# Kernel tuning notes

Hardware: AMD Instinct MI355X
Metric: run time of the kernel (lower is better)

## Reference

```python
import jax, jax.numpy as jnp
import numpy as np

D_MODEL = 1024
D_INNER = 2 * D_MODEL
D_STATE = 16
DT_RANK = (D_MODEL + 15) // 16  # math.ceil(d_model/16) = 64
D_CONV = 4
SEQ_L = 2048
BATCH = 2


def setup_inputs() -> dict:
    key = jax.random.key(0)
    ks = jax.random.split(key, 8)
    def w(k, shape, scale=0.02):
        return jax.random.normal(k, shape, dtype=jnp.float32) * scale
    x = jax.random.normal(ks[0], (SEQ_L, BATCH, D_MODEL), dtype=jnp.float32)
    # weights stored as (in, out); torch Linear is x @ W.T with W (out, in)
    W_in = w(ks[1], (D_MODEL, 2 * D_INNER))
    W_conv = w(ks[2], (D_INNER, 1, D_CONV), 0.3)  # depthwise conv kernel (O, I/groups=1, K)
    b_conv = jnp.zeros((D_INNER,), jnp.float32)
    W_x = w(ks[3], (D_INNER, DT_RANK + 2 * D_STATE))
    W_dt = w(ks[4], (DT_RANK, D_INNER))
    b_dt = jnp.zeros((D_INNER,), jnp.float32)
    A_log = jnp.log(jnp.broadcast_to(jnp.arange(1, D_STATE + 1, dtype=jnp.float32),
                                     (D_INNER, D_STATE)))
    D = jnp.ones((D_INNER,), jnp.float32)
    W_out = w(ks[5], (D_INNER, D_MODEL))
    return {"x": x, "W_in": W_in, "W_conv": W_conv, "b_conv": b_conv,
            "W_x": W_x, "W_dt": W_dt, "b_dt": b_dt,
            "A_log": A_log, "D": D, "W_out": W_out}


def _mamba_forward(x, W_in, W_conv, b_conv, W_x, W_dt, b_dt, A_log, D, W_out):
    xb = jnp.transpose(x, (1, 0, 2))                       # (b, l, d_model)
    b, l, _ = xb.shape
    x_and_res = xb @ W_in                                  # (b, l, 2*d_inner)
    xs, res = jnp.split(x_and_res, 2, axis=-1)
    # depthwise causal conv1d: torch pads d_conv-1 both sides then truncates to l
    xc = jnp.transpose(xs, (0, 2, 1))                      # (b, d_inner, l)
    xc = jax.lax.conv_general_dilated(
        xc, W_conv, window_strides=(1,), padding=[(D_CONV - 1, 0)],
        feature_group_count=D_INNER,
        dimension_numbers=("NCH", "OIH", "NCH")) + b_conv[None, :, None]
    u = jax.nn.silu(jnp.transpose(xc, (0, 2, 1)))          # (b, l, d_inner)
    # SSM parameters
    A = -jnp.exp(A_log)                                    # (d_inner, n)
    x_dbl = u @ W_x                                        # (b, l, dt_rank + 2n)
    delta, Bm, Cm = jnp.split(x_dbl, [DT_RANK, DT_RANK + D_STATE], axis=-1)
    delta = jax.nn.softplus(delta @ W_dt + b_dt)           # (b, l, d_inner)
    # selective scan: state (b, d_inner, n)
    def step(state, inp):
        d_t, B_t, C_t, u_t = inp                           # (b,d_in),(b,n),(b,n),(b,d_in)
        dA = jnp.exp(d_t[:, :, None] * A)                  # (b, d_inner, n)
        dBu = d_t[:, :, None] * B_t[:, None, :] * u_t[:, :, None]
        state = dA * state + dBu
        y_t = jnp.einsum("bdn,bn->bd", state, C_t)
        return state, y_t

    init = jnp.zeros((b, D_INNER, D_STATE), jnp.float32)
    seq = (jnp.moveaxis(delta, 1, 0), jnp.moveaxis(Bm, 1, 0),
           jnp.moveaxis(Cm, 1, 0), jnp.moveaxis(u, 1, 0))
    _, ys = jax.lax.scan(step, init, seq)                  # (l, b, d_inner)
    y = jnp.moveaxis(ys, 0, 1) + u * D                     # (b, l, d_inner)
    y = y * jax.nn.silu(res)
    return y @ W_out                                       # (b, l, d_model)


def reference(x, W_in, W_conv, b_conv, W_x, W_dt, b_dt, A_log, D, W_out):
    return _mamba_forward(x, W_in, W_conv, b_conv, W_x, W_dt, b_dt, A_log, D, W_out)
```

## Files before the change

### kernel.cpp

```cpp
#include <hip/hip_runtime.h>
#include <hip/hip_bf16.h>

#define L_SEQ  2048
#define NBATCH 2
#define DMODEL 1024
#define DINNER 2048
#define DSTATE 16
#define DTRANK 64
#define MROWS  (L_SEQ * NBATCH)
#define NCHUNK 64
#define LCHUNK 32
#define LOG2E  1.44269504f

using bf16 = __hip_bfloat16;
typedef short s16x8 __attribute__((ext_vector_type(8)));
typedef float f32x4 __attribute__((ext_vector_type(4)));

__device__ __forceinline__ void gload_lds16(const bf16* g, bf16* l) {
    __builtin_amdgcn_global_load_lds(
        (const __attribute__((address_space(1))) void*)g,
        (__attribute__((address_space(3))) void*)l, 16, 0, 0);
}

__device__ __forceinline__ float bf2f(short v) {
    return __uint_as_float(((unsigned)(unsigned short)v) << 16);
}

__global__ __launch_bounds__(512, 2)
void gemm256(const bf16* __restrict__ A, const bf16* __restrict__ Bt,
             bf16* __restrict__ C, int N, int K, int lda, int ldb)
{
    __shared__ __align__(16) bf16 As[2][256 * 64];
    __shared__ __align__(16) bf16 Bs[2][256 * 64];

    const int tid  = threadIdx.x;
    const int wid  = tid >> 6;
    const int lane = tid & 63;
    const int wr = wid >> 2, wc = wid & 3;
    const int fr = lane & 15, fk = lane >> 4;

    const int orig = blockIdx.y * gridDim.x + blockIdx.x;
    const int xcd  = orig & 7, k = orig >> 3;
    const int byi  = (xcd >> 1) * 4 + (k >> 3);
    const int bxi  = (xcd & 1) * 8 + (k & 7);
    const long bm = (long)byi * 256;
    const long bn = (long)bxi * 256;

    const int q0 = tid, q1 = tid + 512;
    const int r0 = q0 >> 3, r1 = q1 >> 3;
    const int c0 = ((q0 & 7) ^ (r0 & 7)) << 3;
    const int c1 = ((q1 & 7) ^ (r1 & 7)) << 3;
    const bf16* sA0h0 = A  + (bm + r0)       * (long)lda + c0;
    const bf16* sA1h0 = A  + (bm + r1)       * (long)lda + c1;
    const bf16* sA0h1 = A  + (bm + 128 + r0) * (long)lda + c0;
    const bf16* sA1h1 = A  + (bm + 128 + r1) * (long)lda + c1;
    const bf16* sB0h0 = Bt + (bn + r0)       * (long)ldb + c0;
    const bf16* sB1h0 = Bt + (bn + r1)       * (long)ldb + c1;
    const bf16* sB0h1 = Bt + (bn + 128 + r0) * (long)ldb + c0;
    const bf16* sB1h1 = Bt + (bn + 128 + r1) * (long)ldb + c1;
    const int dst0 = wid * 512;
    const int dst1 = 4096 + wid * 512;

    const int o0   = ((fk ^ (fr & 7)) << 3);
    const int o1   = o0 ^ 32;
    const int rA64 = (wr * 64 + fr) * 64;
    const int rB64 = (wc * 32 + fr) * 64;

    f32x4 acc[8][4] = {};
    s16x8 af[4][2], bf0[2][2], bf1[2][2];
    const int nt = K >> 6;

#define STAGE(ARR, BUF, H, P0, P1) do {                    \
        gload_lds16(P0, &ARR[BUF][(H) * 8192 + dst0]);     \
        gload_lds16(P1, &ARR[BUF][(H) * 8192 + dst1]);     \
        P0 += 64; P1 += 64;                                \
    } while (0)

#define LOADA(MH, CUR) do {                                   \
        const bf16* ab = &As[CUR][rA64 + (MH) * 8192];        \
        _Pragma("unroll") for (int m = 0; m < 4; ++m) {       \
            af[m][0] = *(const s16x8*)&ab[m * 1024 + o0];     \
            af[m][1] = *(const s16x8*)&ab[m * 1024 + o1]; }   \
    } while (0)

#define LOADB(NH, CUR, BF) do {                               \
        const bf16* bb = &Bs[CUR][rB64 + (NH) * 8192];        \
        _Pragma("unroll") for (int n = 0; n < 2; ++n) {       \
            BF[n][0] = *(const s16x8*)&bb[n * 1024 + o0];     \
            BF[n][1] = *(const s16x8*)&bb[n * 1024 + o1]; }   \
    } while (0)

#define MFMAQ(MH, NH, BF) do {                                               \
        __builtin_amdgcn_s_setprio(1);                                       \
        _Pragma("unroll") for (int ks = 0; ks < 2; ++ks)                     \
        _Pragma("unroll") for (int m = 0; m < 4; ++m)                        \
        _Pragma("unroll") for (int n = 0; n < 2; ++n)                        \
            acc[(MH) * 4 + m][(NH) * 2 + n] =                                \
                __builtin_amdgcn_mfma_f32_16x16x32_bf16(                     \
                    af[m][ks], BF[n][ks], acc[(MH) * 4 + m][(NH) * 2 + n],   \
                    0, 0, 0);                                                \
        __builtin_amdgcn_s_setprio(0);                                       \
    } while (0)

#define WB(NV) asm volatile("s_waitcnt vmcnt(" #NV ")\n\ts_barrier" ::: "memory")

    STAGE(As, 0, 0, sA0h0, sA1h0);
    STAGE(Bs, 0, 0, sB0h0, sB1h0);
    STAGE(Bs, 0, 1, sB0h1, sB1h1);
    STAGE(As, 0, 1, sA0h1, sA1h1);

    int cur = 0;
    for (int t = 0; t < nt; ++t) {
        WB(2);
        LOADA(0, cur);
        LOADB(0, cur, bf0);
        LOADB(1, cur, bf1);
        if (t + 1 < nt) {
            STAGE(As, cur ^ 1, 0, sA0h0, sA1h0);
            STAGE(Bs, cur ^ 1, 0, sB0h0, sB1h0);
            STAGE(Bs, cur ^ 1, 1, sB0h1, sB1h1);
            STAGE(As, cur ^ 1, 1, sA0h1, sA1h1);
        }
        MFMAQ(0, 0, bf0);
        MFMAQ(0, 1, bf1);
        if (t + 1 < nt) WB(8); else WB(0);
        LOADA(1, cur);
        MFMAQ(1, 1, bf1);
        MFMAQ(1, 0, bf0);
        cur ^= 1;
    }

#undef STAGE
#undef LOADA
#undef LOADB
#undef MFMAQ
#undef WB

    #pragma unroll
    for (int mh = 0; mh < 2; ++mh)
    #pragma unroll
    for (int m = 0; m < 4; ++m)
    #pragma unroll
    for (int nh = 0; nh < 2; ++nh)
    #pragma unroll
    for (int n = 0; n < 2; ++n) {
        f32x4 v = acc[mh * 4 + m][nh * 2 + n];
        long row0 = bm + wr * 64 + mh * 128 + m * 16 + fk * 4;
        long col  = bn + wc * 32 + nh * 128 + n * 16 + fr;
        #pragma unroll
        for (int j = 0; j < 4; ++j)
            C[(row0 + j) * N + col] = __float2bfloat16(v[j]);
    }
}

template<typename OutT, int EPI, bool SPLITK = false>
__global__ __launch_bounds__(256)
void gemm_bt(const bf16* __restrict__ A, const bf16* __restrict__ Bt,
             OutT* __restrict__ C, const float* __restrict__ bias,
             int M, int N, int K, int lda, int ldb)
{
    __shared__ __align__(16) bf16 As[2][128 * 32];
    __shared__ __align__(16) bf16 Bs[2][128 * 32];

    const int tid  = threadIdx.x;
    const int wave = tid >> 6;
    const int lane = tid & 63;
    const int wr = wave >> 1, wc = wave & 1;
    const int fr = lane & 15, fk = lane >> 4;

    const int nbx = gridDim.x;
    const int nwg = nbx * gridDim.y;
    int id  = blockIdx.y * nbx + blockIdx.x;
    if (nwg >= 8) {
        int cpx = nwg >> 3;
        id = (id & 7) * cpx + (id >> 3);
    }
    const int bxi = id % nbx, byi = id / nbx;
    const long bm = (long)byi * 128;
    const long bn = (long)bxi * 128;

    if constexpr (SPLITK) {
        long ko = (long)blockIdx.z * K;
        A  += ko;
        Bt += ko;
        C  += (size_t)blockIdx.z * M * N;
    }

    const int r0 = tid >> 2,         c0 = (tid & 3) << 3;
    const int r1 = (256 + tid) >> 2, c1 = c0;
    const bf16* pA0 = A  + (bm + r0) * (long)lda + c0;
    const bf16* pA1 = A  + (bm + r1) * (long)lda + c1;
    const bf16* pB0 = Bt + (bn + r0) * (long)ldb + c0;
    const bf16* pB1 = Bt + (bn + r1) * (long)ldb + c1;
    const size_t ld0 = (size_t)(wave * 64) * 8;
    const size_t ld1 = (size_t)(256 + wave * 64) * 8;

    f32x4 acc[4][4] = {};
    const int nt = K >> 5;

#define STG(BUF) do {                             \
        gload_lds16(pA0, &As[BUF][ld0]);          \
        gload_lds16(pB0, &Bs[BUF][ld0]);          \
        gload_lds16(pA1, &As[BUF][ld1]);          \
        gload_lds16(pB1, &Bs[BUF][ld1]);          \
        pA0 += 32; pA1 += 32; pB0 += 32; pB1 += 32; \
    } while (0)

    STG(0);
    if (nt > 1) STG(1);

    int cur = 0;
    for (int t = 0; t < nt; ++t) {
        if (t + 1 < nt)
            asm volatile("s_waitcnt vmcnt(4)\n\ts_barrier" ::: "memory");
        else
            asm volatile("s_waitcnt vmcnt(0)\n\ts_barrier" ::: "memory");

        s16x8 afrag[4], bfrag[4];
        #pragma unroll
        for (int m = 0; m < 4; ++m)
            afrag[m] = *(const s16x8*)&As[cur][(wr * 64 + m * 16 + fr) * 32 + fk * 8];
        #pragma unroll
        for (int n = 0; n < 4; ++n)
            bfrag[n] = *(const s16x8*)&Bs[cur][(wc * 64 + n * 16 + fr) * 32 + fk * 8];

        #pragma unroll
        for (int m = 0; m < 4; ++m)
            #pragma unroll
            for (int n = 0; n < 4; ++n)
                acc[m][n] = __builtin_amdgcn_mfma_f32_16x16x32_bf16(
                    afrag[m], bfrag[n], acc[m][n], 0, 0, 0);

        if (t + 2 < nt) {
            asm volatile("s_waitcnt lgkmcnt(0)\n\ts_barrier" ::: "memory");
            STG(cur);
        }
        cur ^= 1;
    }
#undef STG

    #pragma unroll
    for (int m = 0; m < 4; ++m)
        #pragma unroll
        for (int n = 0; n < 4; ++n) {
            f32x4 v = acc[m][n];
            long row0 = bm + wr * 64 + m * 16 + fk * 4;
            long col  = bn + wc * 64 + n * 16 + fr;
            #pragma unroll
            for (int j = 0; j < 4; ++j) {
                float val = v[j];
                if (EPI == 1) {
                    val += bias[col];
                    val = (val > 20.f) ? val : log1pf(__expf(val));
                }
                if constexpr (sizeof(OutT) == 2)
                    C[(row0 + j) * N + col] = __float2bfloat16(val);
                else
                    C[(row0 + j) * N + col] = val;
            }
        }
}

__device__ __forceinline__ void do_transpose(
    const float* __restrict__ in, bf16* __restrict__ out,
    int R, int C, int Cpad, int bx, int by, int tx, int ty)
{
    __shared__ float tile[32][33];
    int cb = bx * 32, rb = by * 32;
    #pragma unroll
    for (int i = 0; i < 4; ++i) {
        int r = rb + ty + i * 8, c = cb + tx;
        tile[ty + i * 8][tx] = (r < R && c < C) ? in[(long)r * C + c] : 0.f;
    }
    __syncthreads();
    #pragma unroll
    for (int i = 0; i < 4; ++i) {
        int oc = cb + ty + i * 8;
        int orow = rb + tx;
        if (oc < Cpad && orow < R)
            out[(long)oc * R + orow] = __float2bfloat16(tile[tx][ty + i * 8]);
    }
}

__global__ __launch_bounds__(256)
void prep_kernel(const float* __restrict__ W_in,  bf16* __restrict__ WinT,
                 const float* __restrict__ W_x,   bf16* __restrict__ WxT,
                 const float* __restrict__ W_dt,  bf16* __restrict__ WdtT,
                 const float* __restrict__ W_out, bf16* __restrict__ WoutT,
                 const float* __restrict__ x,     bf16* __restrict__ Xb)
{
    const int b  = blockIdx.x;
    const int t  = threadIdx.x;
    const int tx = t & 31, ty = t >> 5;

    if (b < 4096) {
        do_transpose(W_in, WinT, 1024, 4096, 4096, b & 127, b >> 7, tx, ty);
    } else if (b < 4352) {
        int b2 = b - 4096;
        do_transpose(W_x, WxT, 2048, 96, 128, b2 & 3, b2 >> 2, tx, ty);
    } else if (b < 4480) {
        int b3 = b - 4352;
        do_transpose(W_dt, WdtT, 64, 2048, 2048, b3 & 63, b3 >> 6, tx, ty);
    } else if (b < 6528) {
        int b4 = b - 4480;
        do_transpose(W_out, WoutT, 2048, 1024, 1024, b4 & 31, b4 >> 5, tx, ty);
    } else {
        int idx = (b - 6528) * 256 + t;
        int c   = idx & (DMODEL - 1);
        int row = idx >> 10;
        int l   = row & (L_SEQ - 1);
        int bb  = row >> 11;
        Xb[idx] = __float2bfloat16(x[((l * NBATCH + bb) << 10) | c]);
    }
}

__global__ void conv_silu_kernel(const bf16* __restrict__ xr, const float* __restrict__ Wc,
                                 const float* __restrict__ bc, bf16* __restrict__ u)
{
    int idx = blockIdx.x * 256 + threadIdx.x;
    int g   = idx & 255;
    int row = idx >> 8;
    int c   = g << 3;
    int l   = row & (L_SEQ - 1);

    float acc[8];
    f32x4 bi0 = *(const f32x4*)(bc + c);
    f32x4 bi1 = *(const f32x4*)(bc + c + 4);
    #pragma unroll
    for (int j = 0; j < 4; ++j) { acc[j] = bi0[j]; acc[4 + j] = bi1[j]; }

    f32x4 w[8];
    #pragma unroll
    for (int j = 0; j < 8; ++j) w[j] = *(const f32x4*)(Wc + (c + j) * 4);

    #pragma unroll
    for (int t = 0; t < 4; ++t) {
        int ll = l - 3 + t;
        if (ll >= 0) {
            s16x8 v = *(const s16x8*)(xr + (long)(row - 3 + t) * 4096 + c);
            #pragma unroll
            for (int j = 0; j < 8; ++j)
                acc[j] += bf2f(v[j]) * w[j][t];
        }
    }
    s16x8 o;
    #pragma unroll
    for (int j = 0; j < 8; ++j) {
        float a = acc[j];
        float s = a / (1.f + __builtin_amdgcn_exp2f(-LOG2E * a));
        bf16 h = __float2bfloat16(s);
        o[j] = *(short*)&h;
    }
    *(s16x8*)(u + (long)row * DINNER + c) = o;
}

__global__ void reduce_xdbl(const float* __restrict__ part, float* __restrict__ xdbl,
                            bf16* __restrict__ drbf)
{
    int idx = blockIdx.x * 256 + threadIdx.x;
    const size_t stride = (size_t)MROWS * 128;
    float v = part[idx] + part[idx + stride] + part[idx + 2 * stride]
            + part[idx + 3 * stride];
    xdbl[idx] = v;
    int col = idx & 127;
    if (col < 64)
        drbf[(idx >> 7) * 64 + col] = __float2bfloat16(v);
}

__global__ void reduce_out(const float* __restrict__ part, float* __restrict__ out)
{
    int i = blockIdx.x * 256 + threadIdx.x;
    f32x4 a = ((const f32x4*)part)[i];
    f32x4 b = ((const f32x4*)(part + (size_t)MROWS * DMODEL))[i];
    ((f32x4*)out)[i] = a + b;
}

__global__ __launch_bounds__(256)
void scan_phase1(const bf16* __restrict__ delta, const bf16* __restrict__ u,
                 const float* __restrict__ xdbl, const float* __restrict__ A_log,
                 float* __restrict__ AS)
{
    const int idx   = blockIdx.x * 256 + threadIdx.x;
    const int half  = idx & 1;
    const int ch    = idx >> 1;
    const int chunk = blockIdx.y;
    const int d     = ch & (DINNER - 1);
    const int b     = ch >> 11;
    const int n0    = half * 8;

    float A2[8], s[8];
    const f32x4* Arow = (const f32x4*)(A_log + d * DSTATE + n0);
    #pragma unroll
    for (int q = 0; q < 2; ++q) {
        f32x4 v = Arow[q];
        #pragma unroll
        for (int j = 0; j < 4; ++j) A2[q * 4 + j] = -__expf(v[j]) * LOG2E;
    }
    #pragma unroll
    for (int n = 0; n < 8; ++n) s[n] = 0.f;
    float sdl = 0.f;

    bool fastA = true;
    #pragma unroll
    for (int j = 0; j < 8; ++j)
        fastA &= fabsf(A2[j] + (float)(n0 + j + 1) * LOG2E)
                 < 0.01f * (float)(n0 + j + 1);

    const long row0 = (long)b * L_SEQ + chunk * LCHUNK;
    const bf16*  pD = delta + row0 * DINNER + d;
    const bf16*  pU = u     + row0 * DINNER + d;
    const f32x4* pB = (const f32x4*)(xdbl + row0 * 128 + 64 + n0);

    if (fastA) {
        #pragma unroll 4
        for (int l = 0; l < LCHUNK; ++l) {
            float dl = __bfloat162float(*pD);
            float uv = __bfloat162float(*pU);
            f32x4 B0 = pB[0], B1 = pB[1];
            pD += DINNER; pU += DINNER; pB += 32;
            float dbu = dl * uv;
            sdl += dl;
            float b1 = __builtin_amdgcn_exp2f(-LOG2E * dl);
            float b2 = b1 * b1, b3 = b2 * b1, b4 = b2 * b2;
            float b5 = b4 * b1, b6 = b4 * b2, b7 = b4 * b3, b8 = b4 * b4;
            float pre = half ? b8 : 1.f;
            s[0] = pre * b1 * s[0] + dbu * B0[0];
            s[1] = pre * b2 * s[1] + dbu * B0[1];
            s[2] = pre * b3 * s[2] + dbu * B0[2];
            s[3] = pre * b4 * s[3] + dbu * B0[3];
            s[4] = pre * b5 * s[4] + dbu * B1[0];
            s[5] = pre * b6 * s[5] + dbu * B1[1];
            s[6] = pre * b7 * s[6] + dbu * B1[2];
            s[7] = pre * b8 * s[7] + dbu * B1[3];
        }
    } else {
        #pragma unroll 4
        for (int l = 0; l < LCHUNK; ++l) {
            float dl = __bfloat162float(*pD);
            float uv = __bfloat162float(*pU);
            f32x4 B0 = pB[0], B1 = pB[1];
            pD += DINNER; pU += DINNER; pB += 32;
            float dbu = dl * uv;
            sdl += dl;
            #pragma unroll
            for (int j = 0; j < 4; ++j) {
                float e = __builtin_amdgcn_exp2f(dl * A2[j]);
                s[j] = e * s[j] + dbu * B0[j];
            }
            #pragma unroll
            for (int j = 0; j < 4; ++j) {
                float e = __builtin_amdgcn_exp2f(dl * A2[4 + j]);
                s[4 + j] = e * s[4 + j] + dbu * B1[j];
            }
        }
    }
    float ap[8];
    #pragma unroll
    for (int n = 0; n < 8; ++n) ap[n] = __builtin_amdgcn_exp2f(sdl * A2[n]);

    float* o = AS + ((size_t)chunk * 4096 + ch) * 32 + n0;
    *(f32x4*)(o)      = *(f32x4*)&ap[0];
    *(f32x4*)(o + 4)  = *(f32x4*)&ap[4];
    *(f32x4*)(o + 16) = *(f32x4*)&s[0];
    *(f32x4*)(o + 20) = *(f32x4*)&s[4];
}

__global__ __launch_bounds__(256)
void scan_phase2(float* __restrict__ AS)
{
    const int idx = blockIdx.x * 256 + threadIdx.x;
    const int n   = idx & 15;
    const int ch  = idx >> 4;

    float s = 0.f;
    for (int cb = 0; cb < NCHUNK; cb += 16) {
        float av[16], sv[16];
        #pragma unroll
        for (int j = 0; j < 16; ++j) {
            size_t r = ((size_t)(cb + j) * 4096 + ch) * 32 + n;
            av[j] = AS[r];
            sv[j] = AS[r + 16];
        }
        #pragma unroll
        for (int j = 0; j < 16; ++j) {
            AS[((size_t)(cb + j) * 4096 + ch) * 32 + 16 + n] = s;
            s = av[j] * s + sv[j];
        }
    }
}

__global__ __launch_bounds__(256)
void scan_phase3(const bf16* __restrict__ delta, const bf16* __restrict__ u,
                 const float* __restrict__ xdbl, const bf16* __restrict__ xr,
                 const float* __restrict__ AS, const float* __restrict__ A_log,
                 const float* __restrict__ Dp, bf16* __restrict__ ybf)
{
    const int idx   = blockIdx.x * 256 + threadIdx.x;
    const int half  = idx & 1;
    const int ch    = idx >> 1;
    const int chunk = blockIdx.y;
    const int d     = ch & (DINNER - 1);
    const int b     = ch >> 11;
    const int n0    = half * 8;

    float A2[8], s[8];
    const f32x4* Arow = (const f32x4*)(A_log + d * DSTATE + n0);
    #pragma unroll
    for (int q = 0; q < 2; ++q) {
        f32x4 v = Arow[q];
        #pragma unroll
        for (int j = 0; j < 4; ++j) A2[q * 4 + j] = -__expf(v[j]) * LOG2E;
    }
    const float* ip = AS + ((size_t)chunk * 4096 + ch) * 32 + 16 + n0;
    *(f32x4*)&s[0] = *(const f32x4*)(ip);
    *(f32x4*)&s[4] = *(const f32x4*)(ip + 4);

    bool fastA = true;
    #pragma unroll
    for (int j = 0; j < 8; ++j)
        fastA &= fabsf(A2[j] + (float)(n0 + j + 1) * LOG2E)
                 < 0.01f * (float)(n0 + j + 1);

    const float Dd  = Dp[d];
    const long row0 = (long)b * L_SEQ + chunk * LCHUNK;

    const bf16*  pD = delta + row0 * DINNER + d;
    const bf16*  pU = u     + row0 * DINNER + d;
    const bf16*  pR = xr    + row0 * 4096 + 2048 + d;
    const f32x4* pB = (const f32x4*)(xdbl + row0 * 128 + 64 + n0);
    bf16*        pY = ybf   + row0 * DINNER + d;

    if (fastA) {
        #pragma unroll 4
        for (int l = 0; l < LCHUNK; ++l) {
            float dl = __bfloat162float(*pD);
            float uv = __bfloat162float(*pU);
            float rs = __bfloat162float(*pR);
            f32x4 B0 = pB[0], B1 = pB[1];
            f32x4 C0 = pB[4], C1 = pB[5];
            pD += DINNER; pU += DINNER; pR += 4096; pB += 32;
            float dbu = dl * uv;
            float b1 = __builtin_amdgcn_exp2f(-LOG2E * dl);
            float b2 = b1 * b1, b3 = b2 * b1, b4 = b2 * b2;
            float b5 = b4 * b1, b6 = b4 * b2, b7 = b4 * b3, b8 = b4 * b4;
            float pre = half ? b8 : 1.f;
            float y0 = 0.f, y1 = 0.f;
            s[0] = pre * b1 * s[0] + dbu * B0[0];  y0 += s[0] * C0[0];
            s[1] = pre * b2 * s[1] + dbu * B0[1];  y0 += s[1] * C0[1];
            s[2] = pre * b3 * s[2] + dbu * B0[2];  y0 += s[2] * C0[2];
            s[3] = pre * b4 * s[3] + dbu * B0[3];  y0 += s[3] * C0[3];
            s[4] = pre * b5 * s[4] + dbu * B1[0];  y1 += s[4] * C1[0];
            s[5] = pre * b6 * s[5] + dbu * B1[1];  y1 += s[5] * C1[1];
            s[6] = pre * b7 * s[6] + dbu * B1[2];  y1 += s[6] * C1[2];
            s[7] = pre * b8 * s[7] + dbu * B1[3];  y1 += s[7] * C1[3];
            float yh = y0 + y1;
            float yt = yh + __shfl_xor(yh, 1);
            if (half == 0) {
                float yf = yt + uv * Dd;
                yf *= rs / (1.f + __builtin_amdgcn_exp2f(-LOG2E * rs));
                *pY = __float2bfloat16(yf);
            }
            pY += DINNER;
        }
    } else {
        #pragma unroll 4
        for (int l = 0; l < LCHUNK; ++l) {
            float dl = __bfloat162float(*pD);
            float uv = __bfloat162float(*pU);
            float rs = __bfloat162float(*pR);
            f32x4 B0 = pB[0], B1 = pB[1];
            f32x4 C0 = pB[4], C1 = pB[5];
            pD += DINNER; pU += DINNER; pR += 4096; pB += 32;
            float dbu = dl * uv;
            float y0 = 0.f, y1 = 0.f;
            #pragma unroll
            for (int j = 0; j < 4; ++j) {
                float e = __builtin_amdgcn_exp2f(dl * A2[j]);
                s[j] = e * s[j] + dbu * B0[j];
                y0 += s[j] * C0[j];
            }
            #pragma unroll
            for (int j = 0; j < 4; ++j) {
                float e = __builtin_amdgcn_exp2f(dl * A2[4 + j]);
                s[4 + j] = e * s[4 + j] + dbu * B1[j];
                y1 += s[4 + j] * C1[j];
            }
            float yh = y0 + y1;
            float yt = yh + __shfl_xor(yh, 1);
            if (half == 0) {
                float yf = yt + uv * Dd;
                yf *= rs / (1.f + __builtin_amdgcn_exp2f(-LOG2E * rs));
                *pY = __float2bfloat16(yf);
            }
            pY += DINNER;
        }
    }
}

extern "C" void kernel_launch(void* const* d_in, const int* in_sizes, int n_in,
                              void* d_out, int out_size, void* d_ws, size_t ws_size,
                              hipStream_t stream)
{
    const float* x      = (const float*)d_in[0];
    const float* W_in   = (const float*)d_in[1];
    const float* W_conv = (const float*)d_in[2];
    const float* b_conv = (const float*)d_in[3];
    const float* W_x    = (const float*)d_in[4];
    const float* W_dt   = (const float*)d_in[5];
    const float* b_dt   = (const float*)d_in[6];
    const float* A_log  = (const float*)d_in[7];
    const float* Dp     = (const float*)d_in[8];
    const float* W_out  = (const float*)d_in[9];
    float* out = (float*)d_out;

    char* ws = (char*)d_ws;
    size_t off = 0;
    auto alloc = [&](size_t bytes) {
        void* p = ws + off;
        off = (off + bytes + 255) & ~(size_t)255;
        return p;
    };
    bf16*  Xb    = (bf16*) alloc((size_t)MROWS * DMODEL * 2);
    bf16*  WinT  = (bf16*) alloc((size_t)4096  * DMODEL * 2);
    bf16*  xr    = (bf16*) alloc((size_t)MROWS * 4096  * 2);
    bf16*  ubf   = (bf16*) alloc((size_t)MROWS * DINNER * 2);
    bf16*  WxT   = (bf16*) alloc((size_t)128   * DINNER * 2);
    float* xdbl  = (float*)alloc((size_t)MROWS * 128 * 4);
    float* xdblp = (float*)alloc((size_t)4 * MROWS * 128 * 4);
    bf16*  drbf  = (bf16*) alloc((size_t)MROWS * 64 * 2);
    bf16*  WdtT  = (bf16*) alloc((size_t)DINNER * 64 * 2);
    bf16*  delta = (bf16*) alloc((size_t)MROWS * DINNER * 2);
    bf16*  ybf   = (bf16*) alloc((size_t)MROWS * DINNER * 2);
    bf16*  WoutT = (bf16*) alloc((size_t)DMODEL * DINNER * 2);
    float* AS    = (float*)alloc((size_t)NCHUNK * 4096 * 32 * 4);

    prep_kernel<<<6528 + (MROWS * DMODEL) / 256, 256, 0, stream>>>(
        W_in, WinT, W_x, WxT, W_dt, WdtT, W_out, WoutT, x, Xb);

    gemm256<<<dim3(4096 / 256, MROWS / 256), 512, 0, stream>>>(
        Xb, WinT, xr, 4096, 1024, 1024, 1024);
    conv_silu_kernel<<<(MROWS * DINNER / 8) / 256, 256, 0, stream>>>(
        xr, W_conv, b_conv, ubf);
    gemm_bt<float, 0, true><<<dim3(1, MROWS / 128, 4), 256, 0, stream>>>(
        ubf, WxT, xdblp, nullptr, MROWS, 128, 512, 2048, 2048);
    reduce_xdbl<<<(MROWS * 128) / 256, 256, 0, stream>>>(xdblp, xdbl, drbf);
    gemm_bt<bf16, 1><<<dim3(DINNER / 128, MROWS / 128), 256, 0, stream>>>(
        drbf, WdtT, delta, b_dt, MROWS, DINNER, 64, 64, 64);
    scan_phase1<<<dim3(32, NCHUNK), 256, 0, stream>>>(delta, ubf, xdbl, A_log, AS);
    scan_phase2<<<256, 256, 0, stream>>>(AS);
    scan_phase3<<<dim3(32, NCHUNK), 256, 0, stream>>>(delta, ubf, xdbl, xr, AS,
                                                      A_log, Dp, ybf);
    gemm_bt<float, 0, true><<<dim3(DMODEL / 128, MROWS / 128, 2), 256, 0, stream>>>(
        ybf, WoutT, (float*)AS, nullptr, MROWS, DMODEL, 1024, 2048, 2048);
    reduce_out<<<(MROWS * DMODEL) / 1024, 256, 0, stream>>>((float*)AS, out);
}
```

Before: 253.2 us.

## Use 8-wave gemm_bt blocks, deeper split-K for x_proj, drop out_proj split-K

The 128x128 gemm_bt tile is now computed by 512 threads (8 waves), each owning a 32x64 sub-tile with one A and one B LDS load per thread per K step. The x_proj GEMM splits K eight ways instead of four, and reduce_xdbl sums eight partials. The out_proj GEMM no longer uses split-K plus a separate reduce kernel; it writes directly to the output over the full K. The aim is higher per-block parallelism and fewer launches and partial-buffer traffic, at the cost of fewer out_proj blocks and more partial traffic for x_proj.

```diff
diff --git a/kernel.cpp b/kernel.cpp
--- a/kernel.cpp
+++ b/kernel.cpp
@@ -154,7 +154,7 @@
 }
 
 template<typename OutT, int EPI, bool SPLITK = false>
-__global__ __launch_bounds__(256)
+__global__ __launch_bounds__(512)
 void gemm_bt(const bf16* __restrict__ A, const bf16* __restrict__ Bt,
              OutT* __restrict__ C, const float* __restrict__ bias,
              int M, int N, int K, int lda, int ldb)
@@ -163,9 +163,9 @@
     __shared__ __align__(16) bf16 Bs[2][128 * 32];
 
     const int tid  = threadIdx.x;
-    const int wave = tid >> 6;
+    const int wid  = tid >> 6;
     const int lane = tid & 63;
-    const int wr = wave >> 1, wc = wave & 1;
+    const int wr = wid >> 1, wc = wid & 1;
     const int fr = lane & 15, fk = lane >> 4;
 
     const int nbx = gridDim.x;
@@ -186,24 +186,18 @@
         C  += (size_t)blockIdx.z * M * N;
     }
 
-    const int r0 = tid >> 2,         c0 = (tid & 3) << 3;
-    const int r1 = (256 + tid) >> 2, c1 = c0;
-    const bf16* pA0 = A  + (bm + r0) * (long)lda + c0;
-    const bf16* pA1 = A  + (bm + r1) * (long)lda + c1;
-    const bf16* pB0 = Bt + (bn + r0) * (long)ldb + c0;
-    const bf16* pB1 = Bt + (bn + r1) * (long)ldb + c1;
-    const size_t ld0 = (size_t)(wave * 64) * 8;
-    const size_t ld1 = (size_t)(256 + wave * 64) * 8;
-
-    f32x4 acc[4][4] = {};
+    const int r0 = tid >> 2, c0 = (tid & 3) << 3;
+    const bf16* pA = A  + (bm + r0) * (long)lda + c0;
+    const bf16* pB = Bt + (bn + r0) * (long)ldb + c0;
+    const size_t ld = (size_t)wid * 512;
+
+    f32x4 acc[2][4] = {};
     const int nt = K >> 5;
 
 #define STG(BUF) do {                             \
-        gload_lds16(pA0, &As[BUF][ld0]);          \
-        gload_lds16(pB0, &Bs[BUF][ld0]);          \
-        gload_lds16(pA1, &As[BUF][ld1]);          \
-        gload_lds16(pB1, &Bs[BUF][ld1]);          \
-        pA0 += 32; pA1 += 32; pB0 += 32; pB1 += 32; \
+        gload_lds16(pA, &As[BUF][ld]);            \
+        gload_lds16(pB, &Bs[BUF][ld]);            \
+        pA += 32; pB += 32;                       \
     } while (0)
 
     STG(0);
@@ -212,20 +206,20 @@
     int cur = 0;
     for (int t = 0; t < nt; ++t) {
         if (t + 1 < nt)
-            asm volatile("s_waitcnt vmcnt(4)\n\ts_barrier" ::: "memory");
+            asm volatile("s_waitcnt vmcnt(2)\n\ts_barrier" ::: "memory");
         else
             asm volatile("s_waitcnt vmcnt(0)\n\ts_barrier" ::: "memory");
 
-        s16x8 afrag[4], bfrag[4];
-        #pragma unroll
-        for (int m = 0; m < 4; ++m)
-            afrag[m] = *(const s16x8*)&As[cur][(wr * 64 + m * 16 + fr) * 32 + fk * 8];
+        s16x8 afrag[2], bfrag[4];
+        #pragma unroll
+        for (int m = 0; m < 2; ++m)
+            afrag[m] = *(const s16x8*)&As[cur][(wr * 32 + m * 16 + fr) * 32 + fk * 8];
         #pragma unroll
         for (int n = 0; n < 4; ++n)
             bfrag[n] = *(const s16x8*)&Bs[cur][(wc * 64 + n * 16 + fr) * 32 + fk * 8];
 
         #pragma unroll
-        for (int m = 0; m < 4; ++m)
+        for (int m = 0; m < 2; ++m)
             #pragma unroll
             for (int n = 0; n < 4; ++n)
                 acc[m][n] = __builtin_amdgcn_mfma_f32_16x16x32_bf16(
@@ -240,11 +234,11 @@
 #undef STG
 
     #pragma unroll
-    for (int m = 0; m < 4; ++m)
+    for (int m = 0; m < 2; ++m)
         #pragma unroll
         for (int n = 0; n < 4; ++n) {
             f32x4 v = acc[m][n];
-            long row0 = bm + wr * 64 + m * 16 + fk * 4;
+            long row0 = bm + wr * 32 + m * 16 + fk * 4;
             long col  = bn + wc * 64 + n * 16 + fr;
             #pragma unroll
             for (int j = 0; j < 4; ++j) {
@@ -359,20 +353,14 @@
 {
     int idx = blockIdx.x * 256 + threadIdx.x;
     const size_t stride = (size_t)MROWS * 128;
-    float v = part[idx] + part[idx + stride] + part[idx + 2 * stride]
-            + part[idx + 3 * stride];
+    float v = 0.f;
+    #pragma unroll
+    for (int z = 0; z < 8; ++z)
+        v += part[idx + z * stride];
     xdbl[idx] = v;
     int col = idx & 127;
     if (col < 64)
         drbf[(idx >> 7) * 64 + col] = __float2bfloat16(v);
-}
-
-__global__ void reduce_out(const float* __restrict__ part, float* __restrict__ out)
-{
-    int i = blockIdx.x * 256 + threadIdx.x;
-    f32x4 a = ((const f32x4*)part)[i];
-    f32x4 b = ((const f32x4*)(part + (size_t)MROWS * DMODEL))[i];
-    ((f32x4*)out)[i] = a + b;
 }
 
 __global__ __launch_bounds__(256)
@@ -626,7 +614,7 @@
     bf16*  ubf   = (bf16*) alloc((size_t)MROWS * DINNER * 2);
     bf16*  WxT   = (bf16*) alloc((size_t)128   * DINNER * 2);
     float* xdbl  = (float*)alloc((size_t)MROWS * 128 * 4);
-    float* xdblp = (float*)alloc((size_t)4 * MROWS * 128 * 4);
+    float* xdblp = (float*)alloc((size_t)8 * MROWS * 128 * 4);
     bf16*  drbf  = (bf16*) alloc((size_t)MROWS * 64 * 2);
     bf16*  WdtT  = (bf16*) alloc((size_t)DINNER * 64 * 2);
     bf16*  delta = (bf16*) alloc((size_t)MROWS * DINNER * 2);
@@ -641,16 +629,15 @@
         Xb, WinT, xr, 4096, 1024, 1024, 1024);
     conv_silu_kernel<<<(MROWS * DINNER / 8) / 256, 256, 0, stream>>>(
         xr, W_conv, b_conv, ubf);
-    gemm_bt<float, 0, true><<<dim3(1, MROWS / 128, 4), 256, 0, stream>>>(
-        ubf, WxT, xdblp, nullptr, MROWS, 128, 512, 2048, 2048);
+    gemm_bt<float, 0, true><<<dim3(1, MROWS / 128, 8), 512, 0, stream>>>(
+        ubf, WxT, xdblp, nullptr, MROWS, 128, 256, 2048, 2048);
     reduce_xdbl<<<(MROWS * 128) / 256, 256, 0, stream>>>(xdblp, xdbl, drbf);
-    gemm_bt<bf16, 1><<<dim3(DINNER / 128, MROWS / 128), 256, 0, stream>>>(
+    gemm_bt<bf16, 1><<<dim3(DINNER / 128, MROWS / 128), 512, 0, stream>>>(
         drbf, WdtT, delta, b_dt, MROWS, DINNER, 64, 64, 64);
     scan_phase1<<<dim3(32, NCHUNK), 256, 0, stream>>>(delta, ubf, xdbl, A_log, AS);
     scan_phase2<<<256, 256, 0, stream>>>(AS);
     scan_phase3<<<dim3(32, NCHUNK), 256, 0, stream>>>(delta, ubf, xdbl, xr, AS,
                                                       A_log, Dp, ybf);
-    gemm_bt<float, 0, true><<<dim3(DMODEL / 128, MROWS / 128, 2), 256, 0, stream>>>(
-        ybf, WoutT, (float*)AS, nullptr, MROWS, DMODEL, 1024, 2048, 2048);
-    reduce_out<<<(MROWS * DMODEL) / 1024, 256, 0, stream>>>((float*)AS, out);
-}
+    gemm_bt<float, 0><<<dim3(DMODEL / 128, MROWS / 128), 512, 0, stream>>>(
+        ybf, WoutT, out, nullptr, MROWS, DMODEL, 2048, 2048, 2048);
+}
```

New measurement: 248.2 us, median of 2. -2.0%, faster.
